# Optimization experiments

Measured on AMD Instinct MI355X. Metric: run time of the kernel, lower is better.

## Reference

```python
import jax, jax.numpy as jnp
import numpy as np

N_SRC = 50000; N_DST = 50000; E = 800000
IN_NODE = 128; IN_EDGE = 16; OUT_NODE = 64; OUT_EDGE = 16; H = 4
LEAKY_SLOPE = 0.01  # F.leaky_relu default used inside dgl EGATConv


def setup_inputs() -> dict:
    key = jax.random.key(0)
    ks = jax.random.split(key, 11)
    return dict(
        nfeats=jax.random.normal(ks[0], (N_SRC, IN_NODE), jnp.float32),
        dst_feats=jax.random.normal(ks[1], (N_DST, IN_NODE), jnp.float32),
        reward=jax.random.uniform(ks[2], (E,), jnp.float32),
        src=jax.random.randint(ks[3], (E,), 0, N_SRC),
        dst=jax.random.randint(ks[4], (E,), 0, N_DST),
        W_ns=jax.random.normal(ks[5], (IN_NODE, H * OUT_NODE), jnp.float32) * 0.05,
        b_ns=jnp.zeros((H * OUT_NODE,), jnp.float32),
        W_ni=jax.random.normal(ks[6], (IN_NODE, H * OUT_EDGE), jnp.float32) * 0.05,
        W_nj=jax.random.normal(ks[7], (IN_NODE, H * OUT_EDGE), jnp.float32) * 0.05,
        W_fij=jax.random.normal(ks[8], (IN_EDGE, H * OUT_EDGE), jnp.float32) * 0.05,
        attn=jax.random.normal(ks[9], (H, OUT_EDGE), jnp.float32) * 0.05,
        b_e=jnp.zeros((H * OUT_EDGE,), jnp.float32),
    )


def reference(nfeats, dst_feats, reward, src, dst,
              W_ns, b_ns, W_ni, W_nj, W_fij, attn, b_e):
    # EGAT.forward with num_layers=1: efeats = reward repeated to IN_EDGE cols
    efeats = jnp.repeat(reward[:, None], IN_EDGE, axis=1)              # (E, Fe_in)
    # --- EGATConv ---
    f_ni = nfeats @ W_ni                                               # (Ns, H*Fe)
    f_nj = dst_feats @ W_nj                                            # (Nd, H*Fe)
    f_out = f_ni[src] + f_nj[dst] + efeats @ W_fij + b_e               # (E, H*Fe)
    f_out = jax.nn.leaky_relu(f_out, LEAKY_SLOPE).reshape(E, H, OUT_EDGE)
    e = jnp.einsum('ehf,hf->eh', f_out, attn)                          # (E, H)
    # edge softmax over incoming edges of each dst node (stable)
    m = jax.ops.segment_max(e, dst, num_segments=N_DST)                # (Nd, H)
    a = jnp.exp(e - m[dst])
    s = jax.ops.segment_sum(a, dst, num_segments=N_DST)                # (Nd, H)
    a = a / jnp.where(s > 0, s, 1.0)[dst]                              # (E, H)
    # weighted aggregation of projected src features
    h_src = (nfeats @ W_ns + b_ns).reshape(N_SRC, H, OUT_NODE)
    msg = h_src[src] * a[:, :, None]                                   # (E, H, Fn)
    h_out = jax.ops.segment_sum(msg, dst, num_segments=N_DST)          # (Nd, H, Fn)
    # wrapper: mean over heads then ReLU
    return jax.nn.relu(h_out.mean(axis=1))                             # (Nd, Fn)
```

## Files before the change

### kernel.cpp

```cpp
#include <hip/hip_runtime.h>

#define IN_NODE 128
#define OUT_NODE 64
#define NHEAD 4
#define HN 256
#define HE 64
#define LEAKY 0.01f
#define DPW 8

typedef __attribute__((ext_vector_type(8))) short bf16x8;
typedef __attribute__((ext_vector_type(4))) float f32x4;
typedef __attribute__((ext_vector_type(2))) float f32x2;

__device__ __forceinline__ float bf2f(unsigned short u) {
    union { unsigned u; float f; } v; v.u = ((unsigned)u) << 16; return v.f;
}
__device__ __forceinline__ unsigned short f2bf(float x) {
    union { float f; unsigned u; } v; v.f = x;
    unsigned r = v.u + 0x7FFF + ((v.u >> 16) & 1);
    return (unsigned short)(r >> 16);
}
__device__ __forceinline__ bf16x8 cvt8(float4 a, float4 b) {
    bf16x8 r;
    r[0] = (short)f2bf(a.x); r[1] = (short)f2bf(a.y);
    r[2] = (short)f2bf(a.z); r[3] = (short)f2bf(a.w);
    r[4] = (short)f2bf(b.x); r[5] = (short)f2bf(b.y);
    r[6] = (short)f2bf(b.z); r[7] = (short)f2bf(b.w);
    return r;
}
__device__ __forceinline__ f32x2 bfcvt2(unsigned d) {
    union { unsigned u; float f; } lo, hi;
    lo.u = d << 16; hi.u = d & 0xFFFF0000u;
    f32x2 r; r.x = lo.f; r.y = hi.f; return r;
}

__global__ void prep_hist(const float* __restrict__ W_fij,
                          const float* __restrict__ W_ni,
                          const float* __restrict__ W_ns,
                          const float* __restrict__ W_nj,
                          const int* __restrict__ dst,
                          float* __restrict__ wsum, unsigned short* __restrict__ WT,
                          int* __restrict__ cnt, int E) {
    int b = blockIdx.x;
    if (b == 0) {
        int k = threadIdx.x;
        if (k < 64) {
            float s = 0.f;
#pragma unroll
            for (int c = 0; c < 16; ++c) s += W_fij[c * 64 + k];
            wsum[k] = s;
        }
        return;
    }
    if (b <= 12) {
        int base = (b - 1) * 4096 + threadIdx.x;
#pragma unroll
        for (int i = 0; i < 16; ++i) {
            int idx = base + i * 256;
            int g   = idx >> 11;
            int rem = idx & 2047;
            int c   = rem >> 9;
            int l   = (rem >> 3) & 63;
            int j   = rem & 7;
            int nl  = l & 15;
            int k   = c * 32 + (l >> 4) * 8 + j;
            unsigned short v;
            if (g < 4)       v = f2bf(W_ni[k * 64  + g * 16 + nl]);
            else if (g < 20) v = f2bf(W_ns[k * 256 + (g - 4) * 16 + nl]);
            else             v = f2bf(W_nj[k * 64  + (g - 20) * 16 + nl]);
            WT[idx] = v;
        }
        return;
    }
    int i = (b - 13) * 256 + threadIdx.x;
    if (i < E) atomicAdd(&cnt[dst[i]], 1);
}

__global__ __launch_bounds__(256) void scan_all(const int* __restrict__ cnt,
                                                int* __restrict__ row_ptr,
                                                int* __restrict__ partials,
                                                int* __restrict__ flags,
                                                int n, int E, int nb) {
    __shared__ int sums[256];
    __shared__ int s_base;
    int tid = threadIdx.x, b = blockIdx.x;
    int base = b * 1024;
    int v[4]; int tsum = 0;
#pragma unroll
    for (int j = 0; j < 4; ++j) {
        int idx = base + tid * 4 + j;
        v[j] = (idx < n) ? cnt[idx] : 0;
        tsum += v[j];
    }
    sums[tid] = tsum;
    __syncthreads();
    for (int off = 1; off < 256; off <<= 1) {
        int x = (tid >= off) ? sums[tid - off] : 0;
        __syncthreads();
        sums[tid] += x;
        __syncthreads();
    }
    if (tid == 255) {
        __hip_atomic_store(&partials[b], sums[255], __ATOMIC_RELAXED, __HIP_MEMORY_SCOPE_AGENT);
        __hip_atomic_store(&flags[b], 1, __ATOMIC_RELEASE, __HIP_MEMORY_SCOPE_AGENT);
    }
    if (tid < 64) {
        int val = 0;
        if (tid < nb) {
            while (__hip_atomic_load(&flags[tid], __ATOMIC_ACQUIRE, __HIP_MEMORY_SCOPE_AGENT) == 0) {
                __builtin_amdgcn_s_sleep(1);
            }
            val = __hip_atomic_load(&partials[tid], __ATOMIC_RELAXED, __HIP_MEMORY_SCOPE_AGENT);
        }
#pragma unroll
        for (int o = 1; o < 64; o <<= 1) {
            int x = __shfl_up(val, o);
            if (tid >= o) val += x;
        }
        int off = (b > 0) ? __shfl(val, b - 1) : 0;
        if (tid == 0) s_base = off;
    }
    __syncthreads();
    int run = s_base + sums[tid] - tsum;
#pragma unroll
    for (int j = 0; j < 4; ++j) {
        int idx = base + tid * 4 + j;
        if (idx < n) row_ptr[idx] = run;
        run += v[j];
    }
    if (b == nb - 1 && tid == 0) row_ptr[n] = E;
}

template<int NG, int G0>
__device__ __forceinline__ void gemm_tile(
    const float* __restrict__ A, int rowBase, int M,
    const unsigned short* __restrict__ WB, const float* __restrict__ b_ns,
    unsigned short* __restrict__ f_ni, unsigned short* __restrict__ h_src,
    unsigned short* __restrict__ f_nj, unsigned short* As)
{
    const int t = threadIdx.x;
    const float4* A4 = reinterpret_cast<const float4*>(A);
#pragma unroll
    for (int j = 0; j < 4; ++j) {
        int gi = j * 256 + t;
        int r  = gi >> 4;
        int gr = rowBase + r; if (gr >= M) gr = M - 1;
        int fi = (gi & 15) * 2;
        float4 a0 = A4[(size_t)gr * 32 + fi];
        float4 a1 = A4[(size_t)gr * 32 + fi + 1];
        int byteoff = (gi * 16) ^ ((r & 7) << 4);
        *reinterpret_cast<bf16x8*>(reinterpret_cast<char*>(As) + byteoff) = cvt8(a0, a1);
    }
    __syncthreads();

    const int lane = t & 63, w = t >> 6;
    const int rw = rowBase + w * 16;
    if (rw >= M) return;
    const int m = lane & 15, q = lane >> 4;
    const int tr = w * 16 + m;

    f32x4 acc[NG] = {};
    const char* Asb = reinterpret_cast<const char*>(As);
#pragma unroll
    for (int c = 0; c < 4; ++c) {
        int gi  = tr * 16 + c * 4 + q;
        int off = (gi * 16) ^ ((tr & 7) << 4);
        bf16x8 af = *reinterpret_cast<const bf16x8*>(Asb + off);
#pragma unroll
        for (int g = 0; g < NG; ++g) {
            bf16x8 bf = *reinterpret_cast<const bf16x8*>(
                WB + (size_t)(((G0 + g) * 4 + c) * 64 + lane) * 8);
            acc[g] = __builtin_amdgcn_mfma_f32_16x16x32_bf16(af, bf, acc[g], 0, 0, 0);
        }
    }

#pragma unroll
    for (int g = 0; g < NG; ++g) {
        const int ga = G0 + g;
        unsigned short* C; int N, colBase; const float* bias = nullptr;
        if (ga < 4)       { C = f_ni;  N = 64;  colBase = ga * 16; }
        else if (ga < 20) { C = h_src; N = 256; colBase = (ga - 4) * 16; bias = b_ns; }
        else              { C = f_nj;  N = 64;  colBase = (ga - 20) * 16; }
        int col = colBase + m;
        float bv = bias ? bias[col] : 0.f;
#pragma unroll
        for (int rr = 0; rr < 4; ++rr) {
            int orow = rw + q * 4 + rr;
            if (orow < M) C[(size_t)orow * N + col] = f2bf(acc[g][rr] + bv);
        }
    }
}

__global__ __launch_bounds__(256) void mega(
    const float* __restrict__ nfeats, const float* __restrict__ dst_feats,
    const unsigned short* __restrict__ WT, const float* __restrict__ b_ns,
    const int* __restrict__ src, const int* __restrict__ dst,
    const float* __restrict__ reward, const int* __restrict__ row_ptr,
    int* __restrict__ cnt,
    unsigned short* __restrict__ f_ni, unsigned short* __restrict__ h_src,
    unsigned short* __restrict__ f_nj, int2* __restrict__ sr_s,
    int Ns, int Nd, int E, int nBlkNf, int nBlkDj, int nScatter)
{
    __shared__ __align__(16) unsigned short As[64 * 128];
    const int g = blockIdx.x / 3, r = blockIdx.x % 3;
    if (r == 0) {
        if (g < nBlkNf) {
            gemm_tile<20, 0>(nfeats, g * 64, Ns, WT, b_ns, f_ni, h_src, f_nj, As);
        } else if (g < nBlkNf + nBlkDj) {
            gemm_tile<4, 20>(dst_feats, (g - nBlkNf) * 64, Nd, WT, b_ns, f_ni, h_src, f_nj, As);
        }
        return;
    }
    const int sb = g * 2 + (r - 1);
    if (sb >= nScatter) return;
    int i = sb * 256 + threadIdx.x;
    if (i >= E) return;
    int d = dst[i];
    int pos = row_ptr[d] + atomicSub(&cnt[d], 1) - 1;
    sr_s[pos] = make_int2(src[i], __float_as_int(reward[i]));
}

struct G { uint2 ui; uint4 h0; uint4 h1; };
__device__ __forceinline__ G gatherE(const unsigned short* __restrict__ f_ni,
                                     const unsigned short* __restrict__ h_src,
                                     int sn, int ll, int hq) {
    G g;
    g.ui = *reinterpret_cast<const uint2*>(f_ni + (size_t)sn * HE + 4 * ll);
    const unsigned short* hp = h_src + (size_t)sn * HN + hq;
    g.h0 = *reinterpret_cast<const uint4*>(hp);
    g.h1 = *reinterpret_cast<const uint4*>(hp + 8);
    return g;
}

__global__ __launch_bounds__(256) void fused_agg(
    const unsigned short* __restrict__ f_ni, const unsigned short* __restrict__ f_nj,
    const unsigned short* __restrict__ h_src, const int2* __restrict__ sr_s,
    const int* __restrict__ row_ptr,
    const float* __restrict__ wsum, const float* __restrict__ b_e,
    const float* __restrict__ attn, float* __restrict__ out, int Nd)
{
    __shared__ float red[4][1024];
    const int wv = threadIdx.x >> 6, lane = threadIdx.x & 63;
    const int gw = blockIdx.x * 4 + wv;
    const int ll = lane & 15, sub = lane >> 4;
    const int hq = ((lane >> 2) & 3) * 64 + (lane & 3) * 16;

    int d0 = gw * DPW;
    if (d0 >= Nd) return;
    int d1 = d0 + DPW; if (d1 > Nd) d1 = Nd;

    float4 wsv = *reinterpret_cast<const float4*>(wsum + 4 * ll);
    float4 bev = *reinterpret_cast<const float4*>(b_e + 4 * ll);
    float4 atv = *reinterpret_cast<const float4*>(attn + 4 * ll);
    f32x2 ws01 = {wsv.x, wsv.y}, ws23 = {wsv.z, wsv.w};
    f32x2 at01 = {atv.x, atv.y}, at23 = {atv.z, atv.w};
    const f32x2 lk2 = {LEAKY, LEAKY};

    int nextBeg = row_ptr[d0];
    for (int d = d0; d < d1; ++d) {
        const int beg = nextBeg;
        const int end = row_ptr[d + 1];
        nextBeg = end;
        const int deg = end - beg;

        float den = 0.f;
        f32x2 a0 = {}, a1 = {}, a2 = {}, a3 = {}, a4 = {}, a5 = {}, a6 = {}, a7 = {};

        if (deg > 0) {
            uint2 uj = *reinterpret_cast<const uint2*>(f_nj + (size_t)d * HE + 4 * ll);
            f32x2 bb01 = bfcvt2(uj.x) + (f32x2){bev.x, bev.y};
            f32x2 bb23 = bfcvt2(uj.y) + (f32x2){bev.z, bev.w};
            const int nq = (deg + 3) >> 2;
            const int last = end - 1;

#define LDSR(q) ({ int qq_ = ((q) < nq) ? (q) : (nq - 1);                 \
                   int slot_ = beg + qq_ * 4 + sub;                       \
                   if (slot_ > last) slot_ = last;                        \
                   sr_s[slot_]; })

#define COMPUTE(sr, gg, kq) do {                                          \
    float r_ = __int_as_float((sr).y);                                    \
    f32x2 r2_ = {r_, r_};                                                 \
    f32x2 v01_ = bfcvt2((gg).ui.x) + r2_ * ws01 + bb01;                   \
    f32x2 v23_ = bfcvt2((gg).ui.y) + r2_ * ws23 + bb23;                   \
    v01_ = __builtin_elementwise_max(v01_, v01_ * lk2);                   \
    v23_ = __builtin_elementwise_max(v23_, v23_ * lk2);                   \
    f32x2 t2_ = v01_ * at01 + v23_ * at23;                                \
    float t_ = t2_.x + t2_.y;                                             \
    t_ += __shfl_xor(t_, 1);                                              \
    t_ += __shfl_xor(t_, 2);                                              \
    float ev_ = ((beg + (kq) * 4 + sub) < end) ? __expf(t_) : 0.f;        \
    den += ev_;                                                           \
    f32x2 ev2_ = {ev_, ev_};                                              \
    a0 += bfcvt2((gg).h0.x) * ev2_;                                       \
    a1 += bfcvt2((gg).h0.y) * ev2_;                                       \
    a2 += bfcvt2((gg).h0.z) * ev2_;                                       \
    a3 += bfcvt2((gg).h0.w) * ev2_;                                       \
    a4 += bfcvt2((gg).h1.x) * ev2_;                                       \
    a5 += bfcvt2((gg).h1.y) * ev2_;                                       \
    a6 += bfcvt2((gg).h1.z) * ev2_;                                       \
    a7 += bfcvt2((gg).h1.w) * ev2_;                                       \
} while (0)

            int2 sr0 = LDSR(0), sr1 = LDSR(1), sr2 = LDSR(2);
            G gA = gatherE(f_ni, h_src, sr0.x, ll, hq);
            G gB = gatherE(f_ni, h_src, sr1.x, ll, hq);
            for (int k = 0; k < nq; k += 2) {
                int2 sr3 = LDSR(k + 3);
                G gC = gatherE(f_ni, h_src, sr2.x, ll, hq);
                COMPUTE(sr0, gA, k);
                int2 sr4 = LDSR(k + 4);
                G gD = gatherE(f_ni, h_src, sr3.x, ll, hq);
                if (k + 1 < nq) COMPUTE(sr1, gB, k + 1);
                sr0 = sr2; sr1 = sr3; sr2 = sr4; gA = gC; gB = gD;
            }
#undef COMPUTE
#undef LDSR
        }

        den += __shfl_xor(den, 16);
        den += __shfl_xor(den, 32);
        float sc = (den > 0.f) ? 0.25f / den : 0.f;
        float* wr = &red[wv][sub * 256 + hq];
        float4 s0 = {a0.x * sc, a0.y * sc, a1.x * sc, a1.y * sc};
        float4 s1 = {a2.x * sc, a2.y * sc, a3.x * sc, a3.y * sc};
        float4 s2 = {a4.x * sc, a4.y * sc, a5.x * sc, a5.y * sc};
        float4 s3 = {a6.x * sc, a6.y * sc, a7.x * sc, a7.y * sc};
        *reinterpret_cast<float4*>(wr)      = s0;
        *reinterpret_cast<float4*>(wr + 4)  = s1;
        *reinterpret_cast<float4*>(wr + 8)  = s2;
        *reinterpret_cast<float4*>(wr + 12) = s3;
        asm volatile("s_waitcnt lgkmcnt(0)" ::: "memory");
        float ssum = 0.f;
        const float* rd = &red[wv][lane];
#pragma unroll
        for (int s = 0; s < 4; ++s)
#pragma unroll
            for (int h = 0; h < 4; ++h)
                ssum += rd[s * 256 + h * 64];
        out[(size_t)d * OUT_NODE + lane] = fmaxf(ssum, 0.f);
    }
}

static inline char* align256(char* p) {
    return (char*)(((uintptr_t)p + 255) & ~(uintptr_t)255);
}

extern "C" void kernel_launch(void* const* d_in, const int* in_sizes, int n_in,
                              void* d_out, int out_size, void* d_ws, size_t ws_size,
                              hipStream_t stream) {
    const float* nfeats    = (const float*)d_in[0];
    const float* dst_feats = (const float*)d_in[1];
    const float* reward    = (const float*)d_in[2];
    const int*   src       = (const int*)d_in[3];
    const int*   dst       = (const int*)d_in[4];
    const float* W_ns      = (const float*)d_in[5];
    const float* b_ns      = (const float*)d_in[6];
    const float* W_ni      = (const float*)d_in[7];
    const float* W_nj      = (const float*)d_in[8];
    const float* W_fij     = (const float*)d_in[9];
    const float* attn      = (const float*)d_in[10];
    const float* b_e       = (const float*)d_in[11];
    float* out = (float*)d_out;

    const int Ns = in_sizes[0] / IN_NODE;
    const int Nd = in_sizes[1] / IN_NODE;
    const int E  = in_sizes[2];

    char* ws = (char*)d_ws;
    unsigned short* f_ni  = (unsigned short*)ws; ws = align256(ws + (size_t)Ns * HE * 2);
    unsigned short* f_nj  = (unsigned short*)ws; ws = align256(ws + (size_t)Nd * HE * 2);
    unsigned short* h_src = (unsigned short*)ws; ws = align256(ws + (size_t)Ns * HN * 2);
    unsigned short* WT    = (unsigned short*)ws; ws = align256(ws + 49152 * 2);
    float* wsum    = (float*)ws; ws = align256(ws + HE * 4);
    int*   cnt     = (int*)ws;
    int*   flags   = cnt + Nd;   ws = align256(ws + (size_t)(Nd + 64) * 4);
    int*   row_ptr = (int*)ws;   ws = align256(ws + (size_t)(Nd + 1) * 4);
    int*   partials= (int*)ws;   ws = align256(ws + 256 * 4);
    int2*  sr_s    = (int2*)ws;  ws = align256(ws + (size_t)E * 8);

    hipMemsetAsync(cnt, 0, (size_t)(Nd + 64) * 4, stream);

    prep_hist<<<13 + (E + 255) / 256, 256, 0, stream>>>(
        W_fij, W_ni, W_ns, W_nj, dst, wsum, WT, cnt, E);

    int nb = (Nd + 1023) / 1024;
    scan_all<<<nb, 256, 0, stream>>>(cnt, row_ptr, partials, flags, Nd, E, nb);

    int nBlkNf = (Ns + 63) / 64;
    int nBlkDj = (Nd + 63) / 64;
    int nG = nBlkNf + nBlkDj;
    int nScatter = (E + 255) / 256;
    int nGroups = (nG > (nScatter + 1) / 2) ? nG : (nScatter + 1) / 2;
    mega<<<nGroups * 3, 256, 0, stream>>>(
        nfeats, dst_feats, WT, b_ns, src, dst, reward, row_ptr, cnt,
        f_ni, h_src, f_nj, sr_s, Ns, Nd, E, nBlkNf, nBlkDj, nScatter);

    int nWavesF = (Nd + DPW - 1) / DPW;
    int nBlocksF = (nWavesF + 3) / 4;
    fused_agg<<<nBlocksF, 256, 0, stream>>>(
        f_ni, f_nj, h_src, sr_s, row_ptr, wsum, b_e, attn, out, Nd);
}
```

Measured before the change: 279.4 us.

## Use atomic work-stealing for aggregation waves with persistent grid and swizzled LDS reduce

```diff
diff --git a/kernel.cpp b/kernel.cpp
--- a/kernel.cpp
+++ b/kernel.cpp
@@ -6,7 +6,7 @@
 #define HN 256
 #define HE 64
 #define LEAKY 0.01f
-#define DPW 8
+#define DPB 4
 
 typedef __attribute__((ext_vector_type(8))) short bf16x8;
 typedef __attribute__((ext_vector_type(4))) float f32x4;
@@ -237,17 +237,14 @@
     const unsigned short* __restrict__ h_src, const int2* __restrict__ sr_s,
     const int* __restrict__ row_ptr,
     const float* __restrict__ wsum, const float* __restrict__ b_e,
-    const float* __restrict__ attn, float* __restrict__ out, int Nd)
+    const float* __restrict__ attn, int* __restrict__ wkctr,
+    float* __restrict__ out, int Nd)
 {
     __shared__ float red[4][1024];
     const int wv = threadIdx.x >> 6, lane = threadIdx.x & 63;
-    const int gw = blockIdx.x * 4 + wv;
     const int ll = lane & 15, sub = lane >> 4;
     const int hq = ((lane >> 2) & 3) * 64 + (lane & 3) * 16;
-
-    int d0 = gw * DPW;
-    if (d0 >= Nd) return;
-    int d1 = d0 + DPW; if (d1 > Nd) d1 = Nd;
+    const int mql = (lane >> 1) & 3;
 
     float4 wsv = *reinterpret_cast<const float4*>(wsum + 4 * ll);
     float4 bev = *reinterpret_cast<const float4*>(b_e + 4 * ll);
@@ -256,22 +253,31 @@
     f32x2 at01 = {atv.x, atv.y}, at23 = {atv.z, atv.w};
     const f32x2 lk2 = {LEAKY, LEAKY};
 
-    int nextBeg = row_ptr[d0];
-    for (int d = d0; d < d1; ++d) {
-        const int beg = nextBeg;
-        const int end = row_ptr[d + 1];
-        nextBeg = end;
-        const int deg = end - beg;
-
-        float den = 0.f;
-        f32x2 a0 = {}, a1 = {}, a2 = {}, a3 = {}, a4 = {}, a5 = {}, a6 = {}, a7 = {};
-
-        if (deg > 0) {
-            uint2 uj = *reinterpret_cast<const uint2*>(f_nj + (size_t)d * HE + 4 * ll);
-            f32x2 bb01 = bfcvt2(uj.x) + (f32x2){bev.x, bev.y};
-            f32x2 bb23 = bfcvt2(uj.y) + (f32x2){bev.z, bev.w};
-            const int nq = (deg + 3) >> 2;
-            const int last = end - 1;
+    int curB;
+    if (lane == 0) curB = atomicAdd(wkctr, DPB);
+    curB = __shfl(curB, 0);
+
+    while (curB < Nd) {
+        int nxt_;
+        if (lane == 0) nxt_ = atomicAdd(wkctr, DPB);
+
+        int dEnd = curB + DPB; if (dEnd > Nd) dEnd = Nd;
+        int nextBeg = row_ptr[curB];
+        for (int d = curB; d < dEnd; ++d) {
+            const int beg = nextBeg;
+            const int end = row_ptr[d + 1];
+            nextBeg = end;
+            const int deg = end - beg;
+
+            float den = 0.f;
+            f32x2 a0 = {}, a1 = {}, a2 = {}, a3 = {}, a4 = {}, a5 = {}, a6 = {}, a7 = {};
+
+            if (deg > 0) {
+                uint2 uj = *reinterpret_cast<const uint2*>(f_nj + (size_t)d * HE + 4 * ll);
+                f32x2 bb01 = bfcvt2(uj.x) + (f32x2){bev.x, bev.y};
+                f32x2 bb23 = bfcvt2(uj.y) + (f32x2){bev.z, bev.w};
+                const int nq = (deg + 3) >> 2;
+                const int last = end - 1;
 
 #define LDSR(q) ({ int qq_ = ((q) < nq) ? (q) : (nq - 1);                 \
                    int slot_ = beg + qq_ * 4 + sub;                       \
@@ -302,43 +308,45 @@
     a7 += bfcvt2((gg).h1.w) * ev2_;                                       \
 } while (0)
 
-            int2 sr0 = LDSR(0), sr1 = LDSR(1), sr2 = LDSR(2);
-            G gA = gatherE(f_ni, h_src, sr0.x, ll, hq);
-            G gB = gatherE(f_ni, h_src, sr1.x, ll, hq);
-            for (int k = 0; k < nq; k += 2) {
-                int2 sr3 = LDSR(k + 3);
-                G gC = gatherE(f_ni, h_src, sr2.x, ll, hq);
-                COMPUTE(sr0, gA, k);
-                int2 sr4 = LDSR(k + 4);
-                G gD = gatherE(f_ni, h_src, sr3.x, ll, hq);
-                if (k + 1 < nq) COMPUTE(sr1, gB, k + 1);
-                sr0 = sr2; sr1 = sr3; sr2 = sr4; gA = gC; gB = gD;
-            }
+                int2 sr0 = LDSR(0), sr1 = LDSR(1);
+                G gA = gatherE(f_ni, h_src, sr0.x, ll, hq);
+                for (int k = 0; k < nq; ++k) {
+                    int2 sr2 = LDSR(k + 2);
+                    G gB = gatherE(f_ni, h_src, sr1.x, ll, hq);
+                    COMPUTE(sr0, gA, k);
+                    sr0 = sr1; sr1 = sr2; gA = gB;
+                }
 #undef COMPUTE
 #undef LDSR
-        }
-
-        den += __shfl_xor(den, 16);
-        den += __shfl_xor(den, 32);
-        float sc = (den > 0.f) ? 0.25f / den : 0.f;
-        float* wr = &red[wv][sub * 256 + hq];
-        float4 s0 = {a0.x * sc, a0.y * sc, a1.x * sc, a1.y * sc};
-        float4 s1 = {a2.x * sc, a2.y * sc, a3.x * sc, a3.y * sc};
-        float4 s2 = {a4.x * sc, a4.y * sc, a5.x * sc, a5.y * sc};
-        float4 s3 = {a6.x * sc, a6.y * sc, a7.x * sc, a7.y * sc};
-        *reinterpret_cast<float4*>(wr)      = s0;
-        *reinterpret_cast<float4*>(wr + 4)  = s1;
-        *reinterpret_cast<float4*>(wr + 8)  = s2;
-        *reinterpret_cast<float4*>(wr + 12) = s3;
-        asm volatile("s_waitcnt lgkmcnt(0)" ::: "memory");
-        float ssum = 0.f;
-        const float* rd = &red[wv][lane];
-#pragma unroll
-        for (int s = 0; s < 4; ++s)
-#pragma unroll
-            for (int h = 0; h < 4; ++h)
-                ssum += rd[s * 256 + h * 64];
-        out[(size_t)d * OUT_NODE + lane] = fmaxf(ssum, 0.f);
+            }
+
+            den += __shfl_xor(den, 16);
+            den += __shfl_xor(den, 32);
+            float sc = (den > 0.f) ? 0.25f / den : 0.f;
+            float* wr = &red[wv][lane * 16];
+            float4 s0 = {a0.x * sc, a0.y * sc, a1.x * sc, a1.y * sc};
+            float4 s1 = {a2.x * sc, a2.y * sc, a3.x * sc, a3.y * sc};
+            float4 s2 = {a4.x * sc, a4.y * sc, a5.x * sc, a5.y * sc};
+            float4 s3 = {a6.x * sc, a6.y * sc, a7.x * sc, a7.y * sc};
+            *reinterpret_cast<float4*>(wr + ((0 ^ mql) << 2)) = s0;
+            *reinterpret_cast<float4*>(wr + ((1 ^ mql) << 2)) = s1;
+            *reinterpret_cast<float4*>(wr + ((2 ^ mql) << 2)) = s2;
+            *reinterpret_cast<float4*>(wr + ((3 ^ mql) << 2)) = s3;
+            asm volatile("s_waitcnt lgkmcnt(0)" ::: "memory");
+            float ssum = 0.f;
+            const int e = lane & 15, c45 = lane >> 4;
+#pragma unroll
+            for (int s = 0; s < 4; ++s)
+#pragma unroll
+                for (int h = 0; h < 4; ++h) {
+                    int L = s * 16 + h * 4 + c45;
+                    int m2 = (L >> 1) & 3;
+                    int fi = L * 16 + (((e >> 2) ^ m2) << 2) + (e & 3);
+                    ssum += red[wv][fi];
+                }
+            out[(size_t)d * OUT_NODE + lane] = fmaxf(ssum, 0.f);
+        }
+        curB = __shfl(nxt_, 0);
     }
 }
 
@@ -374,12 +382,13 @@
     unsigned short* WT    = (unsigned short*)ws; ws = align256(ws + 49152 * 2);
     float* wsum    = (float*)ws; ws = align256(ws + HE * 4);
     int*   cnt     = (int*)ws;
-    int*   flags   = cnt + Nd;   ws = align256(ws + (size_t)(Nd + 64) * 4);
+    int*   flags   = cnt + Nd;
+    int*   wkctr   = cnt + Nd + 64; ws = align256(ws + (size_t)(Nd + 65) * 4);
     int*   row_ptr = (int*)ws;   ws = align256(ws + (size_t)(Nd + 1) * 4);
     int*   partials= (int*)ws;   ws = align256(ws + 256 * 4);
     int2*  sr_s    = (int2*)ws;  ws = align256(ws + (size_t)E * 8);
 
-    hipMemsetAsync(cnt, 0, (size_t)(Nd + 64) * 4, stream);
+    hipMemsetAsync(cnt, 0, (size_t)(Nd + 65) * 4, stream);
 
     prep_hist<<<13 + (E + 255) / 256, 256, 0, stream>>>(
         W_fij, W_ni, W_ns, W_nj, dst, wsum, WT, cnt, E);
@@ -396,8 +405,6 @@
         nfeats, dst_feats, WT, b_ns, src, dst, reward, row_ptr, cnt,
         f_ni, h_src, f_nj, sr_s, Ns, Nd, E, nBlkNf, nBlkDj, nScatter);
 
-    int nWavesF = (Nd + DPW - 1) / DPW;
-    int nBlocksF = (nWavesF + 3) / 4;
-    fused_agg<<<nBlocksF, 256, 0, stream>>>(
-        f_ni, f_nj, h_src, sr_s, row_ptr, wsum, b_e, attn, out, Nd);
-}
+    fused_agg<<<2048, 256, 0, stream>>>(
+        f_ni, f_nj, h_src, sr_s, row_ptr, wsum, b_e, attn, wkctr, out, Nd);
+}
```

After: 479.7 us. 1.72x slower.
